# Kernel tuning notes

Measured on AMD Instinct MI355X. Metric: run time of the kernel, lower is better.

The kernel has to match this reference:

```python
import jax, jax.numpy as jnp
import numpy as np
from jax.ops import segment_sum

N = 100000
E = 1600000
D_IN = 64
D_H = 64
D_OUT = 16


def _gcn_norm(edge_index, n_nodes):
    # PyG GCNConv default: add self-loops, symmetric normalization.
    src, dst = edge_index[0], edge_index[1]
    loop = jnp.arange(n_nodes, dtype=edge_index.dtype)
    src = jnp.concatenate([src, loop])
    dst = jnp.concatenate([dst, loop])
    deg = segment_sum(jnp.ones(src.shape[0], dtype=jnp.float32), dst, num_segments=n_nodes)
    dinv = jnp.where(deg > 0, jax.lax.rsqrt(deg), 0.0)
    norm = dinv[src] * dinv[dst]  # [E + N]
    return src, dst, norm


def _gcn_layer(x, W, b, src, dst, norm, n_nodes):
    h = x @ W  # dense transform first (out_channels <= in_channels)
    msg = h[src] * norm[:, None]          # gather + scale  [E+N, out]
    agg = segment_sum(msg, dst, num_segments=n_nodes)  # scatter-add
    return agg + b


def setup_inputs() -> dict:
    key = jax.random.key(0)
    ks = jax.random.split(key, 10)
    x = jax.random.normal(ks[0], (N, D_IN), dtype=jnp.float32)
    edge_index = jax.random.randint(ks[1], (2, E), 0, N, dtype=jnp.int64)

    def glorot(k, fan_in, fan_out):
        lim = np.sqrt(6.0 / (fan_in + fan_out)).astype(np.float32)
        return jax.random.uniform(k, (fan_in, fan_out), jnp.float32, -lim, lim)

    return {
        "x": x,
        "edge_index": edge_index,
        "W1": glorot(ks[2], D_IN, D_H), "b1": jnp.zeros((D_H,), jnp.float32),
        "W2": glorot(ks[3], D_H, D_H), "b2": jnp.zeros((D_H,), jnp.float32),
        "W3": glorot(ks[4], D_H, D_H), "b3": jnp.zeros((D_H,), jnp.float32),
        "W4": glorot(ks[5], D_H, D_OUT), "b4": jnp.zeros((D_OUT,), jnp.float32),
    }


def reference(x, edge_index, W1, b1, W2, b2, W3, b3, W4, b4):
    n = x.shape[0]
    src, dst, norm = _gcn_norm(edge_index, n)
    h = jax.nn.relu(_gcn_layer(x, W1, b1, src, dst, norm, n))
    h = jax.nn.relu(_gcn_layer(h, W2, b2, src, dst, norm, n))
    h = jax.nn.relu(_gcn_layer(h, W3, b3, src, dst, norm, n))
    return _gcn_layer(h, W4, b4, src, dst, norm, n)
```

## Files before the change

kernel.cpp:

```cpp
#include <hip/hip_runtime.h>
#include <hip/hip_fp16.h>

#define NN 100000
#define NE 1600000
#define BK 512
#define BKSH 9
#define NBKT 196
#define SRCMASK 0x1FFFF

typedef _Float16 half2v __attribute__((ext_vector_type(2)));

__device__ inline float dot2acc(unsigned int a, unsigned int b, float c) {
#if __has_builtin(__builtin_amdgcn_fdot2)
    union { unsigned int u; half2v h; } ua, ub;
    ua.u = a; ub.u = b;
    return __builtin_amdgcn_fdot2(ua.h, ub.h, c, false);
#else
    float2 fa = __half22float2(*(const __half2*)&a);
    float2 fb = __half22float2(*(const __half2*)&b);
    return c + fa.x * fb.x + fa.y * fb.y;
#endif
}

__device__ inline int wave_incl_scan(int v, int lane) {
#pragma unroll
    for (int off = 1; off < 64; off <<= 1) {
        int t = __shfl_up(v, off, 64);
        if (lane >= off) v += t;
    }
    return v;
}


__global__ __launch_bounds__(256) void zero_small_kernel(int* __restrict__ p, int n) {
    int i = threadIdx.x + blockIdx.x * 256;
    if (i < n) p[i] = 0;
}

__global__ __launch_bounds__(256) void bhist_kernel(const int* __restrict__ dst,
                                                    int* __restrict__ bcnt, int e) {
    __shared__ int h[4 * NBKT];
    int tid = threadIdx.x;
    int wv = tid >> 6;
    for (int i = tid; i < 4 * NBKT; i += 256) h[i] = 0;
    __syncthreads();
    for (int i = blockIdx.x * 256 + tid; i < e; i += gridDim.x * 256)
        atomicAdd(&h[wv * NBKT + (__builtin_nontemporal_load(&dst[i]) >> BKSH)], 1);
    __syncthreads();
    for (int i = tid; i < NBKT; i += 256) {
        int s = h[i] + h[NBKT + i] + h[2 * NBKT + i] + h[3 * NBKT + i];
        if (s) atomicAdd(&bcnt[i], s);
    }
}

__global__ __launch_bounds__(256) void bscan_kernel(const int* __restrict__ bcnt,
                                                    int* __restrict__ bbase,
                                                    int* __restrict__ bcur) {
    __shared__ int sc[256];
    int tid = threadIdx.x;
    int v = (tid < NBKT) ? bcnt[tid] : 0;
    sc[tid] = v;
    __syncthreads();
    for (int off = 1; off < 256; off <<= 1) {
        int t2 = (tid >= off) ? sc[tid - off] : 0;
        __syncthreads();
        sc[tid] += t2;
        __syncthreads();
    }
    if (tid < NBKT) {
        int ex = sc[tid] - v;
        bbase[tid] = ex;
        bcur[tid] = ex;
    }
    if (tid == 255) bbase[NBKT] = sc[255];
}

__global__ __launch_bounds__(256) void bscatter_kernel(const int* __restrict__ src,
                                                       const int* __restrict__ dst,
                                                       int* __restrict__ bcur,
                                                       unsigned int* __restrict__ bedges,
                                                       int e) {
    __shared__ int h[256];
    __shared__ int sc[256];
    __shared__ int gb[NBKT];
    __shared__ int wsum[4];
    __shared__ int wexc[4];
    __shared__ int2 stg[2048];
    int tid = threadIdx.x, lane = tid & 63, wv = tid >> 6;
    int tile = blockIdx.x * 2048;
    int cnt_tile = min(2048, e - tile);
    h[tid] = 0;
    __syncthreads();
    unsigned int pk[8]; int rk[8], bk[8];
#pragma unroll
    for (int j = 0; j < 8; j++) {
        int li = tid + j * 256;
        if (li < cnt_tile) {
            int s = src[tile + li];
            int d = dst[tile + li];
            bk[j] = d >> BKSH;
            pk[j] = ((unsigned)(d & (BK - 1)) << 17) | (unsigned)s;
            rk[j] = atomicAdd(&h[bk[j]], 1);
        } else bk[j] = -1;
    }
    __syncthreads();
    int v = h[tid];
    int incl = wave_incl_scan(v, lane);
    if (lane == 63) wsum[wv] = incl;
    __syncthreads();
    if (tid == 0) {
        int r = 0;
#pragma unroll
        for (int q = 0; q < 4; q++) { wexc[q] = r; r += wsum[q]; }
    }
    __syncthreads();
    int excl = incl - v + wexc[wv];
    sc[tid] = excl;
    if (tid < NBKT && v > 0) gb[tid] = atomicAdd(&bcur[tid], v);
    __syncthreads();
#pragma unroll
    for (int j = 0; j < 8; j++)
        if (bk[j] >= 0) stg[sc[bk[j]] + rk[j]] = make_int2((int)pk[j], bk[j]);
    __syncthreads();
#pragma unroll
    for (int j = 0; j < 8; j++) {
        int li = tid + j * 256;
        if (li < cnt_tile) {
            int2 p2 = stg[li];
            bedges[gb[p2.y] + (li - sc[p2.y])] = (unsigned int)p2.x;
        }
    }
}

__global__ __launch_bounds__(512) void bfill_kernel(const unsigned int* __restrict__ bedges,
                                                    const int* __restrict__ bbase,
                                                    int* __restrict__ start,
                                                    int* __restrict__ cnt,
                                                    float* __restrict__ dinv,
                                                    int* __restrict__ csr) {
    __shared__ int lcnt[BK];
    __shared__ int lcur[BK];
    __shared__ int wsum[8];
    __shared__ int wexc[8];
    int q = blockIdx.x, tid = threadIdx.x, lane = tid & 63, wv = tid >> 6;
    int ebase = bbase[q], ec = bbase[q + 1] - ebase;
    int nbase = q * BK;
    lcnt[tid] = 0;
    __syncthreads();
    for (int i = tid; i < ec; i += 512)
        atomicAdd(&lcnt[__builtin_nontemporal_load(&bedges[ebase + i]) >> 17], 1);
    __syncthreads();
    int v = lcnt[tid];
    int incl = wave_incl_scan(v, lane);
    if (lane == 63) wsum[wv] = incl;
    __syncthreads();
    if (tid == 0) {
        int r = 0;
#pragma unroll
        for (int p = 0; p < 8; p++) { wexc[p] = r; r += wsum[p]; }
    }
    __syncthreads();
    int ex = incl - v + wexc[wv];
    lcur[tid] = ex;
    int nd = nbase + tid;
    if (nd < NN) {
        start[nd] = ebase + ex;
        cnt[nd]   = v;
        dinv[nd]  = rsqrtf((float)v + 1.0f);
    }
    __syncthreads();
    for (int i = tid; i < ec; i += 512) {
        unsigned int pk = __builtin_nontemporal_load(&bedges[ebase + i]);
        int r = atomicAdd(&lcur[pk >> 17], 1);
        csr[ebase + r] = (int)(pk & SRCMASK);
    }
}

__global__ __launch_bounds__(256) void prep_kernel(const float* __restrict__ x,
                                                   const float* __restrict__ dinv,
                                                   __half* __restrict__ g) {
    size_t i4 = (size_t)blockIdx.x * 256 + threadIdx.x;
    if (i4 >= (size_t)NN * 16) return;
    int row = (int)(i4 >> 4);
    float dv = dinv[row];
    float4 v = *(const float4*)&x[i4 * 4];
    __half2 h01 = __floats2half2_rn(v.x * dv, v.y * dv);
    __half2 h23 = __floats2half2_rn(v.z * dv, v.w * dv);
    __half2* gp = (__half2*)&g[i4 * 4];
    gp[0] = h01;
    gp[1] = h23;
}

__global__ __launch_bounds__(512) void fused_layer_kernel(const __half* __restrict__ g,
                                                          const int* __restrict__ csr,
                                                          const int* __restrict__ start,
                                                          const int* __restrict__ cnt,
                                                          const float* __restrict__ dinv,
                                                          const float* __restrict__ Wg,
                                                          const float* __restrict__ bias,
                                                          __half* __restrict__ gout, int n) {
    __shared__ uint4 wpk[8][64];
    __shared__ __half zh[8][64];
    __shared__ float bs[64];
    int tid = threadIdx.x;
    {
        int p = tid >> 6, c = tid & 63;
        float w[8];
#pragma unroll
        for (int i = 0; i < 8; i++) w[i] = Wg[(8 * p + i) * 64 + c];
        union { __half2 h; unsigned int u; } u0, u1, u2, u3;
        u0.h = __floats2half2_rn(w[0], w[1]);
        u1.h = __floats2half2_rn(w[2], w[3]);
        u2.h = __floats2half2_rn(w[4], w[5]);
        u3.h = __floats2half2_rn(w[6], w[7]);
        wpk[p][c] = make_uint4(u0.u, u1.u, u2.u, u3.u);
    }
    if (tid < 64) bs[tid] = bias[tid];
    __syncthreads();

    int wv = tid >> 6, lane = tid & 63;
    int node = blockIdx.x * 8 + wv;
    float acc = 0.f;
    float dv = 0.f;
    if (node < n) {
        int st = __builtin_amdgcn_readfirstlane(start[node]);
        int cn = __builtin_amdgcn_readfirstlane(cnt[node]);
        dv = dinv[node];
        acc = __half2float(g[(size_t)node * 64 + lane]);
        int e = 0;
        for (; e + 7 < cn; e += 8) {
            int u[8]; float a[8];
#pragma unroll
            for (int j = 0; j < 8; j++) u[j] = __builtin_nontemporal_load(&csr[st + e + j]);
#pragma unroll
            for (int j = 0; j < 8; j++) a[j] = __half2float(g[(size_t)u[j] * 64 + lane]);
            acc += ((a[0] + a[1]) + (a[2] + a[3])) + ((a[4] + a[5]) + (a[6] + a[7]));
        }
        for (; e + 3 < cn; e += 4) {
            int u0 = __builtin_nontemporal_load(&csr[st + e + 0]);
            int u1 = __builtin_nontemporal_load(&csr[st + e + 1]);
            int u2 = __builtin_nontemporal_load(&csr[st + e + 2]);
            int u3 = __builtin_nontemporal_load(&csr[st + e + 3]);
            float a0 = __half2float(g[(size_t)u0 * 64 + lane]);
            float a1 = __half2float(g[(size_t)u1 * 64 + lane]);
            float a2 = __half2float(g[(size_t)u2 * 64 + lane]);
            float a3 = __half2float(g[(size_t)u3 * 64 + lane]);
            acc += (a0 + a1) + (a2 + a3);
        }
        for (; e < cn; e++) {
            int u = __builtin_nontemporal_load(&csr[st + e]);
            acc += __half2float(g[(size_t)u * 64 + lane]);
        }
    }
    zh[wv][lane] = __float2half_rn(acc);
    if (node < n) {
        float t = 0.f;
#pragma unroll
        for (int p = 0; p < 8; p++) {
            uint4 wq = wpk[p][lane];
            uint4 zq = *(const uint4*)&zh[wv][p * 8];
            t = dot2acc(zq.x, wq.x, t);
            t = dot2acc(zq.y, wq.y, t);
            t = dot2acc(zq.z, wq.z, t);
            t = dot2acc(zq.w, wq.w, t);
        }
        float o = dv * t + bs[lane];
        o = fmaxf(o, 0.f);
        gout[(size_t)node * 64 + lane] = __float2half_rn(dv * o);
    }
}

__global__ __launch_bounds__(128) void gemm16_kernel(const __half* __restrict__ xin,
                                                     const float* __restrict__ W,
                                                     __half* __restrict__ s, int n) {
    constexpr int DOUT = 16;
    constexpr int ROWS = 128;
    __shared__ float xs[ROWS][65];
    __shared__ float ws[64][DOUT];
    int tid = threadIdx.x;
    int row0 = blockIdx.x * ROWS;
    for (int i = tid; i < 64 * DOUT; i += 128) ws[i / DOUT][i % DOUT] = W[i];
    for (int i = tid; i < ROWS * 16; i += 128) {
        int r = i >> 4, c = (i & 15) * 4;
        float4 v = make_float4(0.f, 0.f, 0.f, 0.f);
        if (row0 + r < n) {
            const __half* hp = xin + (size_t)(row0 + r) * 64 + c;
            float2 f01 = __half22float2(*(const __half2*)hp);
            float2 f23 = __half22float2(*(const __half2*)(hp + 2));
            v = make_float4(f01.x, f01.y, f23.x, f23.y);
        }
        xs[r][c] = v.x; xs[r][c + 1] = v.y; xs[r][c + 2] = v.z; xs[r][c + 3] = v.w;
    }
    __syncthreads();
    int rbase = tid;
    float acc[16];
#pragma unroll
    for (int j = 0; j < 16; j++) acc[j] = 0.f;
    for (int k = 0; k < 64; k++) {
        float xv = xs[rbase][k];
#pragma unroll
        for (int j = 0; j < 4; j++) {
            float4 wv = *(const float4*)&ws[k][j * 4];
            acc[j * 4 + 0] += xv * wv.x;
            acc[j * 4 + 1] += xv * wv.y;
            acc[j * 4 + 2] += xv * wv.z;
            acc[j * 4 + 3] += xv * wv.w;
        }
    }
    int r = row0 + rbase;
    if (r < n) {
        union { ushort u[16]; uint4 q[2]; } pk;
#pragma unroll
        for (int j = 0; j < 16; j++)
            pk.u[j] = __half_as_ushort(__float2half_rn(acc[j]));
        uint4* sp = (uint4*)&s[(size_t)r * DOUT];
        sp[0] = pk.q[0];
        sp[1] = pk.q[1];
    }
}

__global__ __launch_bounds__(256) void agg16_kernel(const __half* __restrict__ s,
                                                    const int* __restrict__ csr,
                                                    const int* __restrict__ start,
                                                    const int* __restrict__ cnt,
                                                    const float* __restrict__ dinv,
                                                    const float* __restrict__ bias,
                                                    float* __restrict__ out, int n) {
    constexpr int D = 16;
    int tid = threadIdx.x;
    int lane = tid & 63;
    int wave = tid >> 6;
    int col = lane % D;
    int grp = lane / D;
    int node = (blockIdx.x * 4 + wave) * 4 + grp;
    if (node >= n) return;
    int st = start[node];
    int cn = cnt[node];
    float acc = __half2float(s[(size_t)node * D + col]);
    int e = 0;
    for (; e + 7 < cn; e += 8) {
        int u[8]; float a[8];
#pragma unroll
        for (int j = 0; j < 8; j++) u[j] = __builtin_nontemporal_load(&csr[st + e + j]);
#pragma unroll
        for (int j = 0; j < 8; j++) a[j] = __half2float(s[(size_t)u[j] * D + col]);
        acc += ((a[0] + a[1]) + (a[2] + a[3])) + ((a[4] + a[5]) + (a[6] + a[7]));
    }
    for (; e + 3 < cn; e += 4) {
        int u0 = __builtin_nontemporal_load(&csr[st + e + 0]);
        int u1 = __builtin_nontemporal_load(&csr[st + e + 1]);
        int u2 = __builtin_nontemporal_load(&csr[st + e + 2]);
        int u3 = __builtin_nontemporal_load(&csr[st + e + 3]);
        float a0 = __half2float(s[(size_t)u0 * D + col]);
        float a1 = __half2float(s[(size_t)u1 * D + col]);
        float a2 = __half2float(s[(size_t)u2 * D + col]);
        float a3 = __half2float(s[(size_t)u3 * D + col]);
        acc += (a0 + a1) + (a2 + a3);
    }
    for (; e < cn; e++) {
        int u = __builtin_nontemporal_load(&csr[st + e]);
        acc += __half2float(s[(size_t)u * D + col]);
    }
    float o = dinv[node] * acc + bias[col];
    __builtin_nontemporal_store(o, out + (size_t)node * D + col);
}


extern "C" void kernel_launch(void* const* d_in, const int* in_sizes, int n_in,
                              void* d_out, int out_size, void* d_ws, size_t ws_size,
                              hipStream_t stream) {
    const float* x  = (const float*)d_in[0];
    const int* ei   = (const int*)d_in[1];
    const float* W1 = (const float*)d_in[2];
    const float* b1 = (const float*)d_in[3];
    const float* W2 = (const float*)d_in[4];
    const float* b2 = (const float*)d_in[5];
    const float* W3 = (const float*)d_in[6];
    const float* b3 = (const float*)d_in[7];
    const float* W4 = (const float*)d_in[8];
    const float* b4 = (const float*)d_in[9];
    const int* src = ei;
    const int* dst = ei + NE;

    char* w = (char*)d_ws;
    float* dinv  = (float*)w;          w += (size_t)NN * 4;
    int* cnt     = (int*)w;            w += (size_t)NN * 4;
    int* start   = (int*)w;            w += (size_t)NN * 4;
    int* bcnt    = (int*)w;            w += (size_t)(NBKT + 4) * 4;
    int* bbase   = (int*)w;            w += (size_t)(NBKT + 4) * 4;
    int* bcur    = (int*)w;            w += (size_t)(NBKT + 4) * 4;
    int* csr     = (int*)w;            w += (size_t)NE * 4;
    __half* gA   = (__half*)w;         w += (size_t)NN * 64 * 2;
    __half* gB   = (__half*)w;         w += (size_t)NN * 64 * 2;
    __half* s4   = (__half*)w;         w += (size_t)NN * 16 * 2;
    unsigned int* bedges = (unsigned int*)w;  w += (size_t)NE * 4;

    zero_small_kernel<<<1, 256, 0, stream>>>(bcnt, NBKT);
    bhist_kernel<<<512, 256, 0, stream>>>(dst, bcnt, NE);
    bscan_kernel<<<1, 256, 0, stream>>>(bcnt, bbase, bcur);
    bscatter_kernel<<<(NE + 2047) / 2048, 256, 0, stream>>>(src, dst, bcur, bedges, NE);
    bfill_kernel<<<NBKT, 512, 0, stream>>>(bedges, bbase, start, cnt, dinv, csr);

    prep_kernel<<<(NN * 16 + 255) / 256, 256, 0, stream>>>(x, dinv, gA);

    const int FB = (NN + 7) / 8;
    fused_layer_kernel<<<FB, 512, 0, stream>>>(gA, csr, start, cnt, dinv, W1, b1, gB, NN);
    fused_layer_kernel<<<FB, 512, 0, stream>>>(gB, csr, start, cnt, dinv, W2, b2, gA, NN);
    fused_layer_kernel<<<FB, 512, 0, stream>>>(gA, csr, start, cnt, dinv, W3, b3, gB, NN);

    const int GB = (NN + 127) / 128;
    const int AB16 = (NN + 15) / 16;
    gemm16_kernel<<<GB, 128, 0, stream>>>(gB, W4, s4, NN);
    agg16_kernel<<<AB16, 256, 0, stream>>>(s4, csr, start, cnt, dinv, b4, (float*)d_out, NN);
}
```

Before: 359.9 us.

## Replace bucket histogram and scan with fixed-capacity bucket slots

```diff
diff --git a/kernel.cpp b/kernel.cpp
--- a/kernel.cpp
+++ b/kernel.cpp
@@ -6,6 +6,7 @@
 #define BK 512
 #define BKSH 9
 #define NBKT 196
+#define SLOT 9216
 #define SRCMASK 0x1FFFF
 
 typedef _Float16 half2v __attribute__((ext_vector_type(2)));
@@ -37,64 +38,24 @@
     if (i < n) p[i] = 0;
 }
 
-__global__ __launch_bounds__(256) void bhist_kernel(const int* __restrict__ dst,
-                                                    int* __restrict__ bcnt, int e) {
-    __shared__ int h[4 * NBKT];
-    int tid = threadIdx.x;
-    int wv = tid >> 6;
-    for (int i = tid; i < 4 * NBKT; i += 256) h[i] = 0;
-    __syncthreads();
-    for (int i = blockIdx.x * 256 + tid; i < e; i += gridDim.x * 256)
-        atomicAdd(&h[wv * NBKT + (__builtin_nontemporal_load(&dst[i]) >> BKSH)], 1);
-    __syncthreads();
-    for (int i = tid; i < NBKT; i += 256) {
-        int s = h[i] + h[NBKT + i] + h[2 * NBKT + i] + h[3 * NBKT + i];
-        if (s) atomicAdd(&bcnt[i], s);
-    }
-}
-
-__global__ __launch_bounds__(256) void bscan_kernel(const int* __restrict__ bcnt,
-                                                    int* __restrict__ bbase,
-                                                    int* __restrict__ bcur) {
-    __shared__ int sc[256];
-    int tid = threadIdx.x;
-    int v = (tid < NBKT) ? bcnt[tid] : 0;
-    sc[tid] = v;
-    __syncthreads();
-    for (int off = 1; off < 256; off <<= 1) {
-        int t2 = (tid >= off) ? sc[tid - off] : 0;
-        __syncthreads();
-        sc[tid] += t2;
-        __syncthreads();
-    }
-    if (tid < NBKT) {
-        int ex = sc[tid] - v;
-        bbase[tid] = ex;
-        bcur[tid] = ex;
-    }
-    if (tid == 255) bbase[NBKT] = sc[255];
-}
-
-__global__ __launch_bounds__(256) void bscatter_kernel(const int* __restrict__ src,
+__global__ __launch_bounds__(512) void bscatter_kernel(const int* __restrict__ src,
                                                        const int* __restrict__ dst,
                                                        int* __restrict__ bcur,
                                                        unsigned int* __restrict__ bedges,
                                                        int e) {
     __shared__ int h[256];
     __shared__ int sc[256];
-    __shared__ int gb[NBKT];
-    __shared__ int wsum[4];
-    __shared__ int wexc[4];
-    __shared__ int2 stg[2048];
-    int tid = threadIdx.x, lane = tid & 63, wv = tid >> 6;
-    int tile = blockIdx.x * 2048;
-    int cnt_tile = min(2048, e - tile);
-    h[tid] = 0;
+    __shared__ int gb[256];
+    __shared__ int2 stg[4096];
+    int tid = threadIdx.x;
+    int tile = blockIdx.x * 4096;
+    int cnt_tile = min(4096, e - tile);
+    if (tid < 256) h[tid] = 0;
     __syncthreads();
     unsigned int pk[8]; int rk[8], bk[8];
 #pragma unroll
     for (int j = 0; j < 8; j++) {
-        int li = tid + j * 256;
+        int li = tid + j * 512;
         if (li < cnt_tile) {
             int s = src[tile + li];
             int d = dst[tile + li];
@@ -104,19 +65,19 @@
         } else bk[j] = -1;
     }
     __syncthreads();
-    int v = h[tid];
-    int incl = wave_incl_scan(v, lane);
-    if (lane == 63) wsum[wv] = incl;
-    __syncthreads();
-    if (tid == 0) {
-        int r = 0;
-#pragma unroll
-        for (int q = 0; q < 4; q++) { wexc[q] = r; r += wsum[q]; }
-    }
-    __syncthreads();
-    int excl = incl - v + wexc[wv];
-    sc[tid] = excl;
-    if (tid < NBKT && v > 0) gb[tid] = atomicAdd(&bcur[tid], v);
+    if (tid < 64) {
+        int b0 = tid * 4;
+        int c0 = h[b0], c1 = h[b0 + 1], c2 = h[b0 + 2], c3 = h[b0 + 3];
+        int s4 = c0 + c1 + c2 + c3;
+        int incl = wave_incl_scan(s4, tid);
+        int base = incl - s4;
+        sc[b0] = base; sc[b0 + 1] = base + c0;
+        sc[b0 + 2] = base + c0 + c1; sc[b0 + 3] = base + c0 + c1 + c2;
+        if (c0) gb[b0] = atomicAdd(&bcur[b0], c0);
+        if (c1) gb[b0 + 1] = atomicAdd(&bcur[b0 + 1], c1);
+        if (c2) gb[b0 + 2] = atomicAdd(&bcur[b0 + 2], c2);
+        if (c3) gb[b0 + 3] = atomicAdd(&bcur[b0 + 3], c3);
+    }
     __syncthreads();
 #pragma unroll
     for (int j = 0; j < 8; j++)
@@ -124,52 +85,53 @@
     __syncthreads();
 #pragma unroll
     for (int j = 0; j < 8; j++) {
-        int li = tid + j * 256;
+        int li = tid + j * 512;
         if (li < cnt_tile) {
             int2 p2 = stg[li];
-            bedges[gb[p2.y] + (li - sc[p2.y])] = (unsigned int)p2.x;
-        }
-    }
-}
-
-__global__ __launch_bounds__(512) void bfill_kernel(const unsigned int* __restrict__ bedges,
-                                                    const int* __restrict__ bbase,
-                                                    int* __restrict__ start,
-                                                    int* __restrict__ cnt,
-                                                    float* __restrict__ dinv,
-                                                    int* __restrict__ csr) {
+            int b = p2.y;
+            bedges[(size_t)b * SLOT + gb[b] + (li - sc[b])] = (unsigned int)p2.x;
+        }
+    }
+}
+
+__global__ __launch_bounds__(1024) void bfill_kernel(const unsigned int* __restrict__ bedges,
+                                                     const int* __restrict__ bcur,
+                                                     int* __restrict__ start,
+                                                     int* __restrict__ cnt,
+                                                     float* __restrict__ dinv,
+                                                     int* __restrict__ csr) {
     __shared__ int lcnt[BK];
+    __shared__ int lstart[BK];
     __shared__ int lcur[BK];
-    __shared__ int wsum[8];
-    __shared__ int wexc[8];
-    int q = blockIdx.x, tid = threadIdx.x, lane = tid & 63, wv = tid >> 6;
-    int ebase = bbase[q], ec = bbase[q + 1] - ebase;
+    int q = blockIdx.x, tid = threadIdx.x;
+    size_t ebase = (size_t)q * SLOT;
+    int ec = bcur[q];
     int nbase = q * BK;
-    lcnt[tid] = 0;
-    __syncthreads();
-    for (int i = tid; i < ec; i += 512)
+    if (tid < BK) lcnt[tid] = 0;
+    __syncthreads();
+    for (int i = tid; i < ec; i += 1024)
         atomicAdd(&lcnt[__builtin_nontemporal_load(&bedges[ebase + i]) >> 17], 1);
     __syncthreads();
-    int v = lcnt[tid];
-    int incl = wave_incl_scan(v, lane);
-    if (lane == 63) wsum[wv] = incl;
-    __syncthreads();
-    if (tid == 0) {
-        int r = 0;
-#pragma unroll
-        for (int p = 0; p < 8; p++) { wexc[p] = r; r += wsum[p]; }
-    }
-    __syncthreads();
-    int ex = incl - v + wexc[wv];
-    lcur[tid] = ex;
-    int nd = nbase + tid;
-    if (nd < NN) {
-        start[nd] = ebase + ex;
-        cnt[nd]   = v;
-        dinv[nd]  = rsqrtf((float)v + 1.0f);
-    }
-    __syncthreads();
-    for (int i = tid; i < ec; i += 512) {
+    if (tid < 64) {
+        int b0 = tid * 8;
+        int c[8]; int s = 0;
+#pragma unroll
+        for (int k = 0; k < 8; k++) { c[k] = lcnt[b0 + k]; s += c[k]; }
+        int incl = wave_incl_scan(s, tid);
+        int run = incl - s;
+#pragma unroll
+        for (int k = 0; k < 8; k++) { lstart[b0 + k] = run; lcur[b0 + k] = run; run += c[k]; }
+    }
+    __syncthreads();
+    if (tid < BK) {
+        int nd = nbase + tid;
+        if (nd < NN) {
+            start[nd] = (int)ebase + lstart[tid];
+            cnt[nd]   = lcnt[tid];
+            dinv[nd]  = rsqrtf((float)lcnt[tid] + 1.0f);
+        }
+    }
+    for (int i = tid; i < ec; i += 1024) {
         unsigned int pk = __builtin_nontemporal_load(&bedges[ebase + i]);
         int r = atomicAdd(&lcur[pk >> 17], 1);
         csr[ebase + r] = (int)(pk & SRCMASK);
@@ -386,20 +348,16 @@
     float* dinv  = (float*)w;          w += (size_t)NN * 4;
     int* cnt     = (int*)w;            w += (size_t)NN * 4;
     int* start   = (int*)w;            w += (size_t)NN * 4;
-    int* bcnt    = (int*)w;            w += (size_t)(NBKT + 4) * 4;
-    int* bbase   = (int*)w;            w += (size_t)(NBKT + 4) * 4;
-    int* bcur    = (int*)w;            w += (size_t)(NBKT + 4) * 4;
-    int* csr     = (int*)w;            w += (size_t)NE * 4;
+    int* bcur    = (int*)w;            w += (size_t)256 * 4;
+    int* csr     = (int*)w;            w += (size_t)NBKT * SLOT * 4;
     __half* gA   = (__half*)w;         w += (size_t)NN * 64 * 2;
     __half* gB   = (__half*)w;         w += (size_t)NN * 64 * 2;
     __half* s4   = (__half*)w;         w += (size_t)NN * 16 * 2;
-    unsigned int* bedges = (unsigned int*)w;  w += (size_t)NE * 4;
-
-    zero_small_kernel<<<1, 256, 0, stream>>>(bcnt, NBKT);
-    bhist_kernel<<<512, 256, 0, stream>>>(dst, bcnt, NE);
-    bscan_kernel<<<1, 256, 0, stream>>>(bcnt, bbase, bcur);
-    bscatter_kernel<<<(NE + 2047) / 2048, 256, 0, stream>>>(src, dst, bcur, bedges, NE);
-    bfill_kernel<<<NBKT, 512, 0, stream>>>(bedges, bbase, start, cnt, dinv, csr);
+    unsigned int* bedges = (unsigned int*)w;  w += (size_t)NBKT * SLOT * 4;
+
+    zero_small_kernel<<<1, 256, 0, stream>>>(bcur, 256);
+    bscatter_kernel<<<(NE + 4095) / 4096, 512, 0, stream>>>(src, dst, bcur, bedges, NE);
+    bfill_kernel<<<NBKT, 1024, 0, stream>>>(bedges, bcur, start, cnt, dinv, csr);
 
     prep_kernel<<<(NN * 16 + 255) / 256, 256, 0, stream>>>(x, dinv, gA);
 
```

Result: faster. 338.8 us (-5.9%).
